# Kernel tuning notes

Hardware: AMD Instinct MI355X
Metric: run time of the kernel (lower is better)

The kernel has to match this reference:

```python
import jax, jax.numpy as jnp
import numpy as np

NBINS = (128, 64, 32)
LOG2PI = float(np.log(2.0 * np.pi))


def _quadratic_spline_stack(x, genes_oi, local_gene_ix, delta, uh, uw):
    """Stack of piecewise-quadratic (piecewise-linear density) splines on [0,1].
    Per split with n heights / n-1 widths (n-1 bins). Returns (outputs, logabsdet)."""
    uh_oi = uh[genes_oi]  # [G, sum(n)]
    uw_oi = uw[genes_oi]  # [G, sum(n-1)]
    outputs = x
    logabsdet = jnp.zeros_like(x)
    oh = ow = od = 0
    for n in NBINS:
        nh, nw = n, n - 1
        uhs = uh_oi[:, oh:oh + nh]
        uws = uw_oi[:, ow:ow + nw]
        ds = delta[:, od:od + nh]
        oh += nh; ow += nw; od += nh
        # per-gene bin widths / locations
        widths_g = jax.nn.softmax(uws, axis=-1)                     # [G, nw]
        bl = jnp.cumsum(widths_g, axis=-1)
        bl = bl.at[:, -1].set(1.0)
        bin_loc_g = jnp.pad(bl, ((0, 0), (1, 0)))                   # [G, nw+1]
        # gather per cut
        w = widths_g[local_gene_ix]                                 # [N, nw]
        loc = bin_loc_g[local_gene_ix]                              # [N, nw+1]
        # per-cut knot heights: gene baseline + cell/gene delta, normalized to unit area
        h_un = jnp.exp(uhs[local_gene_ix] + ds)                     # [N, nh]
        area = jnp.sum(0.5 * (h_un[:, :-1] + h_un[:, 1:]) * w, axis=-1, keepdims=True)
        h = h_un / area                                             # [N, nh]
        seg = 0.5 * (h[:, :-1] + h[:, 1:]) * w                      # bin masses [N, nw]
        left_cdf = jnp.pad(jnp.cumsum(seg, axis=-1)[:, :-1], ((0, 0), (1, 0)))  # [N, nw]
        # locate bin
        bin_idx = jnp.clip(jnp.sum(outputs[:, None] >= loc, axis=-1) - 1, 0, nw - 1)
        gi = bin_idx[:, None]
        loc_l = jnp.take_along_axis(loc, gi, -1)[:, 0]
        w_b = jnp.take_along_axis(w, gi, -1)[:, 0]
        cdf_l = jnp.take_along_axis(left_cdf, gi, -1)[:, 0]
        h_l = jnp.take_along_axis(h, gi, -1)[:, 0]
        h_r = jnp.take_along_axis(h, gi + 1, -1)[:, 0]
        alpha = (outputs - loc_l) / w_b
        outputs = (0.5 * (h_r - h_l) * w_b) * alpha * alpha + h_l * w_b * alpha + cdf_l
        logabsdet = logabsdet + jnp.log(h_l + (h_r - h_l) * alpha)
    return outputs, logabsdet


def setup_inputs() -> dict:
    key = jax.random.key(0)
    ks = jax.random.split(key, 10)
    B, L, G_total, G_oi, C, N = 512, 16, 20000, 500, 224, 200000
    clustering = jax.random.uniform(ks[0], (B, L), dtype=jnp.float32)
    coordinates = jax.random.uniform(ks[1], (N,), dtype=jnp.float32, minval=1e-4, maxval=1.0 - 1e-4)
    genes_oi = jax.random.randint(ks[2], (G_oi,), 0, G_total)
    local_gene_ix = jax.random.randint(ks[3], (N,), 0, G_oi)
    local_cellxgene_ix = jax.random.randint(ks[4], (N,), 0, B * G_oi)
    localcellxgene_ix = jax.random.randint(ks[5], (N,), 0, B * G_total)
    logit_weight = jax.random.normal(ks[6], (G_total, L, C), dtype=jnp.float32) * 0.01
    rho_weight = jax.random.normal(ks[7], (G_total, L), dtype=jnp.float32) * 0.05
    rho_bias = 1e-5 + (1.0 - 1e-5) * jax.random.uniform(ks[8], (G_total,), dtype=jnp.float32)
    k9, k10 = jax.random.split(ks[9])
    unnormalized_heights = jax.random.normal(k9, (G_total, sum(NBINS)), dtype=jnp.float32) * 0.1
    unnormalized_widths = jax.random.normal(k10, (G_total, sum(n - 1 for n in NBINS)), dtype=jnp.float32) * 0.1
    return dict(clustering=clustering, coordinates=coordinates, genes_oi=genes_oi,
                local_gene_ix=local_gene_ix, local_cellxgene_ix=local_cellxgene_ix,
                localcellxgene_ix=localcellxgene_ix, logit_weight=logit_weight,
                rho_weight=rho_weight, rho_bias=rho_bias,
                unnormalized_heights=unnormalized_heights,
                unnormalized_widths=unnormalized_widths)


def reference(clustering, coordinates, genes_oi, local_gene_ix, local_cellxgene_ix,
              localcellxgene_ix, logit_weight, rho_weight, rho_bias,
              unnormalized_heights, unnormalized_widths):
    B = clustering.shape[0]
    G = genes_oi.shape[0]
    n_total_genes = rho_bias.shape[0]
    # Decoder (n_layers=0 -> nn_output = latent)
    lw_oi = logit_weight[genes_oi]                                   # [G, L, C]
    mixture_delta = jnp.einsum('bl,glc->bgc', clustering, lw_oi)     # [B, G, C]
    rho_delta = clustering @ rho_weight.T                            # [B, G_total]
    rho = jax.nn.softmax(jnp.log(rho_bias)[None, :] + rho_delta, axis=-1)
    rho_cuts = rho.reshape(-1)[localcellxgene_ix]                    # [N]
    md_cuts = mixture_delta.reshape(B * G, -1)[local_cellxgene_ix]   # [N, C]
    _, lik_mixture = _quadratic_spline_stack(coordinates, genes_oi, local_gene_ix,
                                             md_cuts, unnormalized_heights, unnormalized_widths)
    lik_overall = jnp.log(rho_cuts) + jnp.log(jnp.float32(n_total_genes))
    elbo = -jnp.sum(lik_mixture + lik_overall)
    # Normal(0, exp(log_scale=0)=1) regularization log-probs
    def normal_logpdf(v):
        return -0.5 * v * v - 0.5 * LOG2PI
    elbo = elbo - jnp.sum(normal_logpdf(lw_oi))
    elbo = elbo - jnp.sum(normal_logpdf(rho_weight[genes_oi]))
    return elbo
```

## Files before the change

### kernel.cpp

```cpp
#include <hip/hip_runtime.h>
#include <cstddef>

#define LOG2PI_F 1.8378770664093453f

__device__ __forceinline__ float wave_sum(float v) {
#pragma unroll
    for (int o = 32; o >= 1; o >>= 1) v += __shfl_xor(v, o, 64);
    return v;
}
__device__ __forceinline__ float wave_max(float v) {
#pragma unroll
    for (int o = 32; o >= 1; o >>= 1) v = fmaxf(v, __shfl_xor(v, o, 64));
    return v;
}
__device__ __forceinline__ float wave_scan_incl(float v, int lane) {
#pragma unroll
    for (int o = 1; o < 64; o <<= 1) {
        float t = __shfl_up(v, o, 64);
        if (lane >= o) v += t;
    }
    return v;
}

__global__ void k_logrb(const float* __restrict__ rho_bias, float* __restrict__ logrb, int G_total) {
    int g = blockIdx.x * blockDim.x + threadIdx.x;
    if (g < G_total) logrb[g] = __logf(rho_bias[g]);
}

__global__ void k_prep_genes(const int* __restrict__ genes_oi,
                             const float* __restrict__ uh, const float* __restrict__ uw,
                             float4* __restrict__ pk, int G_oi) {
    const int g = blockIdx.x;
    const int t = threadIdx.x;
    const int gs = genes_oi[g];
    const float* uhg = uh + (size_t)gs * 224;
    const float* uwg = uw + (size_t)gs * 221;

    const int NH[3] = {128, 64, 32};
    const int OH[3] = {0, 128, 192};
    const int OW[3] = {0, 127, 190};
    const int SO[3] = {0, 128, 191};
#pragma unroll
    for (int lev = 0; lev < 3; ++lev) {
        const int nw = NH[lev] - 1;
        float v0 = (t < nw)      ? uwg[OW[lev] + t]      : -INFINITY;
        float v1 = (t + 64 < nw) ? uwg[OW[lev] + t + 64] : -INFINITY;
        float mx = wave_max(fmaxf(v0, v1));
        float e0 = (t < nw)      ? __expf(v0 - mx) : 0.f;
        float e1 = (t + 64 < nw) ? __expf(v1 - mx) : 0.f;
        float inv = 1.0f / wave_sum(e0 + e1);
        float w0 = e0 * inv, w1 = e1 * inv;
        float i0 = wave_scan_incl(w0, t);
        float tot0 = __shfl(i0, 63, 64);
        float i1 = wave_scan_incl(w1, t) + tot0;
        if (t < nw) {
            float loc = (t == nw - 1) ? 1.0f : i0;
            pk[(size_t)(SO[lev] + t) * G_oi + g] = make_float4(uhg[OH[lev] + t + 1], 0.5f * w0, loc, 0.f);
        }
        if (t + 64 < nw) {
            int j = t + 64;
            float loc = (j == nw - 1) ? 1.0f : i1;
            pk[(size_t)(SO[lev] + j) * G_oi + g] = make_float4(uhg[OH[lev] + j + 1], 0.5f * w1, loc, 0.f);
        }
    }
    if (t == 0) pk[(size_t)127 * G_oi + g] = make_float4(uhg[0], uhg[128], uhg[192], 0.f);
}

__global__ void k_prep_lwT(const int* __restrict__ genes_oi,
                           const float* __restrict__ lw, const float* __restrict__ rw,
                           float* __restrict__ lwT, float* __restrict__ pB) {
    const int g = blockIdx.x;
    const int tid = threadIdx.x;
    const int gs = genes_oi[g];
    const float* src = lw + (size_t)gs * 3584;
    float* dst = lwT + (size_t)g * 3584;
    float acc = 0.f;
    if (tid < 224) {
        float vv[16];
#pragma unroll
        for (int l = 0; l < 16; ++l) {
            float v = src[l * 224 + tid];
            vv[l] = v;
            acc = fmaf(v, v, acc);
        }
        float4* d4 = (float4*)(dst + (size_t)tid * 16);
#pragma unroll
        for (int q = 0; q < 4; ++q)
            d4[q] = make_float4(vv[4 * q + 0], vv[4 * q + 1], vv[4 * q + 2], vv[4 * q + 3]);
    }
    if (tid < 16) { float v = rw[(size_t)gs * 16 + tid]; acc = fmaf(v, v, acc); }
    __shared__ float sm[256];
    sm[tid] = acc;
    __syncthreads();
    for (int o = 128; o > 0; o >>= 1) { if (tid < o) sm[tid] += sm[tid + o]; __syncthreads(); }
    if (tid == 0) pB[g] = 0.5f * sm[0] + 0.5f * LOG2PI_F * (3584.0f + 16.0f);
}

__global__ void k_lse4(const float* __restrict__ clustering, const float* __restrict__ rw,
                       const float* __restrict__ logrb, float* __restrict__ lse,
                       int G_total, int B) {
    const int b0 = blockIdx.x * 4;
    const int tid = threadIdx.x;
    const int nc = min(4, B - b0);

    float cl[4][16];
#pragma unroll
    for (int c = 0; c < 4; ++c) {
        if (c < nc) {
            const float4* c4 = (const float4*)(clustering + (size_t)(b0 + c) * 16);
#pragma unroll
            for (int q = 0; q < 4; ++q) {
                float4 v = c4[q];
                cl[c][4 * q + 0] = v.x; cl[c][4 * q + 1] = v.y;
                cl[c][4 * q + 2] = v.z; cl[c][4 * q + 3] = v.w;
            }
        } else {
#pragma unroll
            for (int l = 0; l < 16; ++l) cl[c][l] = 0.f;
        }
    }

    float m[4], s[4];
#pragma unroll
    for (int c = 0; c < 4; ++c) { m[c] = -INFINITY; s[c] = 0.f; }

    for (int g = tid; g < G_total; g += 256) {
        const float4* r4 = (const float4*)(rw + (size_t)g * 16);
        float4 rv[4];
#pragma unroll
        for (int q = 0; q < 4; ++q) rv[q] = r4[q];
        const float lb = logrb[g];
#pragma unroll
        for (int c = 0; c < 4; ++c) {
            float d = 0.f;
#pragma unroll
            for (int q = 0; q < 4; ++q) {
                d = fmaf(cl[c][4 * q + 0], rv[q].x, d);
                d = fmaf(cl[c][4 * q + 1], rv[q].y, d);
                d = fmaf(cl[c][4 * q + 2], rv[q].z, d);
                d = fmaf(cl[c][4 * q + 3], rv[q].w, d);
            }
            float logit = lb + d;
            float mn = fmaxf(m[c], logit);
            s[c] = s[c] * __expf(m[c] - mn) + __expf(logit - mn);
            m[c] = mn;
        }
    }

    __shared__ float ms[4][256], ss[4][256];
#pragma unroll
    for (int c = 0; c < 4; ++c) { ms[c][tid] = m[c]; ss[c][tid] = s[c]; }
    __syncthreads();
    for (int o = 128; o > 0; o >>= 1) {
        if (tid < o) {
#pragma unroll
            for (int c = 0; c < 4; ++c) {
                float m2 = ms[c][tid + o], s2 = ss[c][tid + o];
                float mn = fmaxf(ms[c][tid], m2);
                ss[c][tid] = ss[c][tid] * __expf(ms[c][tid] - mn) + s2 * __expf(m2 - mn);
                ms[c][tid] = mn;
            }
        }
        __syncthreads();
    }
    if (tid < 4 && tid < nc) lse[b0 + tid] = ms[tid][0] + __logf(ss[tid][0]);
}

__global__ void k_zero(int* __restrict__ p, int n) {
    int i = blockIdx.x * blockDim.x + threadIdx.x;
    if (i < n) p[i] = 0;
}

__global__ void k_hist(const int* __restrict__ lcx, int* __restrict__ counts, int N, int G_oi) {
    int i = blockIdx.x * blockDim.x + threadIdx.x;
    if (i < N) atomicAdd(&counts[(unsigned)lcx[i] % (unsigned)G_oi], 1);
}

__global__ void k_scan(const int* __restrict__ counts, int* __restrict__ offsets,
                       int* __restrict__ cursor, int G_oi) {
    __shared__ int sm[512];
    const int t = threadIdx.x;
    int v = (t < G_oi) ? counts[t] : 0;
    sm[t] = v;
    __syncthreads();
    for (int o = 1; o < 512; o <<= 1) {
        int add = (t >= o) ? sm[t - o] : 0;
        __syncthreads();
        sm[t] += add;
        __syncthreads();
    }
    if (t < G_oi) {
        offsets[t + 1] = sm[t];
        cursor[t] = sm[t] - v;
    }
    if (t == 0) offsets[0] = 0;
}

__global__ void k_scatter(const float* __restrict__ coord, const int* __restrict__ lgix,
                          const int* __restrict__ lcx, const int* __restrict__ lc2,
                          int* __restrict__ cursor,
                          float* __restrict__ xs, int* __restrict__ b1s,
                          int* __restrict__ lc2s, int* __restrict__ ghs, int N, int G_oi) {
    int i = blockIdx.x * blockDim.x + threadIdx.x;
    if (i >= N) return;
    unsigned v = (unsigned)lcx[i];
    unsigned g = v % (unsigned)G_oi;
    int pos = atomicAdd(&cursor[g], 1);
    xs[pos]   = coord[i];
    b1s[pos]  = (int)(v / (unsigned)G_oi);
    lc2s[pos] = lc2[i];
    ghs[pos]  = lgix[i];
}

__launch_bounds__(512, 4)
__global__ void k_main2(const float* __restrict__ xs, const int* __restrict__ b1s,
                        const int* __restrict__ lc2s, const int* __restrict__ ghs,
                        const int* __restrict__ offsets,
                        const float* __restrict__ clustering,
                        const float* __restrict__ lwT,
                        const float4* __restrict__ pk,
                        const float* __restrict__ rw,
                        const float* __restrict__ logrb,
                        const float* __restrict__ lse,
                        float* __restrict__ pA, int G_oi, int G_total) {
    const int g = blockIdx.x;
    const int tid = threadIdx.x;
    const float* lwg = lwT + (size_t)g * 3584;
    const int s = offsets[g], e = offsets[g + 1];
    const float logGt = __logf((float)G_total);
    float acc = 0.f;

    __shared__ int   s_cnt[512];
    __shared__ int   s_cur[512];
    __shared__ float s_x[512];
    __shared__ int2  s_meta[512];
    __shared__ float wsm[8];

    for (int base = s; base < e; base += 512) {
        const int cnt = min(512, e - base);
        const int i = base + tid;
        const bool valid = tid < cnt;
        const int isafe = valid ? i : s;
        float x0   = xs[isafe];
        int   b1_0 = b1s[isafe];
        int   lc2_0= lc2s[isafe];
        int   gh_0 = ghs[isafe];

        s_cnt[tid] = 0;
        __syncthreads();
        if (valid) atomicAdd(&s_cnt[gh_0], 1);
        __syncthreads();
        int v = s_cnt[tid];
        for (int o = 1; o < 512; o <<= 1) {
            int add = (tid >= o) ? s_cnt[tid - o] : 0;
            __syncthreads();
            s_cnt[tid] += add;
            __syncthreads();
        }
        s_cur[tid] = s_cnt[tid] - v;
        __syncthreads();
        if (valid) {
            int pos = atomicAdd(&s_cur[gh_0], 1);
            s_x[pos]    = x0;
            s_meta[pos] = make_int2((b1_0 << 16) | gh_0, lc2_0);
        }
        __syncthreads();
        const int rd = valid ? tid : 0;
        float x  = s_x[rd];
        int2 mt  = s_meta[rd];
        const int gh  = mt.x & 0xffff;
        const int b1  = mt.x >> 16;
        const int lc2 = mt.y;

        float cl[16];
        {
            const float4* c4 = (const float4*)(clustering + (size_t)b1 * 16);
#pragma unroll
            for (int q = 0; q < 4; ++q) {
                float4 vv = c4[q];
                cl[4 * q + 0] = vv.x; cl[4 * q + 1] = vv.y; cl[4 * q + 2] = vv.z; cl[4 * q + 3] = vv.w;
            }
        }
        const float4 uh0 = pk[(size_t)127 * G_oi + gh];
        const float uh0v[3] = {uh0.x, uh0.y, uh0.z};

        float lad = 0.f;
        const int NH[3] = {128, 64, 32};
        const int OH[3] = {0, 128, 192};
        const int SO[3] = {0, 128, 191};
#pragma unroll
        for (int lev = 0; lev < 3; ++lev) {
            const int nw = NH[lev] - 1;
            const float* rowbase = lwg + (size_t)OH[lev] * 16;
            float hp;
            {
                float d = 0.f;
#pragma unroll
                for (int l = 0; l < 16; ++l) d = fmaf(cl[l], rowbase[l], d);
                hp = __expf(uh0v[lev] + d);
            }
            float h_l = hp, h_r = hp, whb = 0.f, loc_l = 0.f, cdf = 0.f, area = 0.f;
            int in = 0;
            const float4* pks = pk + (size_t)SO[lev] * G_oi + gh;
            for (int j = 0; j < nw; ++j) {
                const float* row = rowbase + (size_t)(j + 1) * 16;
                float d = 0.f;
#pragma unroll
                for (int l = 0; l < 16; ++l) d = fmaf(cl[l], row[l], d);
                float4 pkv = *pks;
                pks += G_oi;
                float hn = __expf(pkv.x + d);
                float seg = (hp + hn) * pkv.y;
                bool inJ = (in == j);
                if (inJ) { h_r = hn; whb = pkv.y; }
                bool adv = (x >= pkv.z) && (j < nw - 1);
                if (adv) { cdf += seg; h_l = hn; loc_l = pkv.z; in = j + 1; }
                area += seg;
                hp = hn;
            }
            float inv_area = __builtin_amdgcn_rcpf(area);
            float alpha = (x - loc_l) * 0.5f * __builtin_amdgcn_rcpf(whb);
            float t2 = whb * alpha;
            x = (t2 * fmaf(h_r - h_l, alpha, 2.f * h_l) + cdf) * inv_area;
            lad += __logf(fmaf(h_r - h_l, alpha, h_l)) - __logf(area);
        }

        unsigned b2 = (unsigned)lc2 / (unsigned)G_total;
        unsigned gt = (unsigned)lc2 - b2 * (unsigned)G_total;
        float d2 = 0.f;
        {
            const float4* c24 = (const float4*)(clustering + (size_t)b2 * 16);
            const float4* r4  = (const float4*)(rw + (size_t)gt * 16);
#pragma unroll
            for (int q = 0; q < 4; ++q) {
                float4 a = c24[q], b = r4[q];
                d2 = fmaf(a.x, b.x, d2); d2 = fmaf(a.y, b.y, d2);
                d2 = fmaf(a.z, b.z, d2); d2 = fmaf(a.w, b.w, d2);
            }
        }
        float lik = logrb[gt] + d2 - lse[b2] + logGt;
        if (valid) acc -= (lad + lik);
    }

    acc = wave_sum(acc);
    if ((tid & 63) == 0) wsm[tid >> 6] = acc;
    __syncthreads();
    if (tid == 0) {
        float t = 0.f;
#pragma unroll
        for (int w = 0; w < 8; ++w) t += wsm[w];
        pA[g] = t;
    }
}

__global__ void k_final(const float* __restrict__ pA, const float* __restrict__ pB,
                        float* __restrict__ out, int nA, int nB) {
    const int tid = threadIdx.x;
    float acc = 0.f;
    for (int i = tid; i < nA; i += blockDim.x) acc += pA[i];
    for (int i = tid; i < nB; i += blockDim.x) acc += pB[i];
    __shared__ float sm[256];
    sm[tid] = acc;
    __syncthreads();
    for (int o = 128; o > 0; o >>= 1) { if (tid < o) sm[tid] += sm[tid + o]; __syncthreads(); }
    if (tid == 0) out[0] = sm[0];
}

extern "C" void kernel_launch(void* const* d_in, const int* in_sizes, int n_in,
                              void* d_out, int out_size, void* d_ws, size_t ws_size,
                              hipStream_t stream) {
    const float* clustering        = (const float*)d_in[0];
    const float* coordinates       = (const float*)d_in[1];
    const int*   genes_oi          = (const int*)d_in[2];
    const int*   local_gene_ix     = (const int*)d_in[3];
    const int*   local_cellxgene_ix= (const int*)d_in[4];
    const int*   localcellxgene_ix = (const int*)d_in[5];
    const float* lw                = (const float*)d_in[6];
    const float* rw                = (const float*)d_in[7];
    const float* rho_bias          = (const float*)d_in[8];
    const float* uh                = (const float*)d_in[9];
    const float* uw                = (const float*)d_in[10];

    const int G_total = in_sizes[8];
    const int G_oi    = in_sizes[2];
    const int N       = in_sizes[1];
    const int L       = in_sizes[7] / G_total;
    const int B       = in_sizes[0] / L;

    size_t off = 0;
    char* base = (char*)d_ws;
    auto alloc = [&](size_t nbytes) {
        char* p = base + off;
        off = (off + nbytes + 15) & ~(size_t)15;
        return (void*)p;
    };
    float*  pA      = (float*)alloc(sizeof(float) * (G_oi + 16));
    float*  pB      = (float*)alloc(sizeof(float) * (G_oi + 16));
    float*  lse     = (float*)alloc(sizeof(float) * (B + 16));
    float*  logrb   = (float*)alloc(sizeof(float) * G_total);
    float*  lwT     = (float*)alloc(sizeof(float) * (size_t)G_oi * 3584);
    float4* pk      = (float4*)alloc(sizeof(float4) * (size_t)G_oi * 224);
    int*    counts  = (int*)alloc(sizeof(int) * 512);
    int*    offsets = (int*)alloc(sizeof(int) * 512);
    int*    cursor  = (int*)alloc(sizeof(int) * 512);
    float*  xs      = (float*)alloc(sizeof(float) * N);
    int*    b1s     = (int*)alloc(sizeof(int) * N);
    int*    lc2s    = (int*)alloc(sizeof(int) * N);
    int*    ghs     = (int*)alloc(sizeof(int) * N);
    (void)ws_size;

    const int TPB = 256;
    k_logrb<<<(G_total + TPB - 1) / TPB, TPB, 0, stream>>>(rho_bias, logrb, G_total);
    k_prep_genes<<<G_oi, 64, 0, stream>>>(genes_oi, uh, uw, pk, G_oi);
    k_prep_lwT<<<G_oi, 256, 0, stream>>>(genes_oi, lw, rw, lwT, pB);
    k_lse4<<<(B + 3) / 4, 256, 0, stream>>>(clustering, rw, logrb, lse, G_total, B);
    k_zero<<<2, 256, 0, stream>>>(counts, 512);
    k_hist<<<(N + TPB - 1) / TPB, TPB, 0, stream>>>(local_cellxgene_ix, counts, N, G_oi);
    k_scan<<<1, 512, 0, stream>>>(counts, offsets, cursor, G_oi);
    k_scatter<<<(N + TPB - 1) / TPB, TPB, 0, stream>>>(coordinates, local_gene_ix,
                                                       local_cellxgene_ix, localcellxgene_ix,
                                                       cursor, xs, b1s, lc2s, ghs, N, G_oi);
    k_main2<<<G_oi, 512, 0, stream>>>(xs, b1s, lc2s, ghs, offsets, clustering, lwT, pk,
                                      rw, logrb, lse, pA, G_oi, G_total);
    k_final<<<1, 256, 0, stream>>>(pA, pB, (float*)d_out, G_oi, G_oi);
}
```

Before: 647.6 us.

## Use packed FP32 FMAs, pack scattered cut data, and fuse small kernels

Rewrites the 16-wide dot products in the main spline loop and in the LSE kernel as two-lane `ext_vector_type` FMAs, so the compiler can emit packed FP32 instructions. The scatter step now writes one float4 per cut (x, packed b1/gene index, lc2) instead of four separate arrays, and the main kernel stages those float4s in LDS. Lanes with no cut now skip all work. Separately, the log of `rho_bias` is folded into the histogram kernel, zeroing of the counts moves into `k_prep_genes`, and `k_lse4` is launched later in the stream. The fused `logrb` write assumes N ≥ G_total and the bit packing assumes small index ranges.

```diff
diff --git a/kernel.cpp b/kernel.cpp
--- a/kernel.cpp
+++ b/kernel.cpp
@@ -2,6 +2,8 @@
 #include <cstddef>
 
 #define LOG2PI_F 1.8378770664093453f
+
+typedef float f2 __attribute__((ext_vector_type(2)));
 
 __device__ __forceinline__ float wave_sum(float v) {
 #pragma unroll
@@ -22,16 +24,19 @@
     return v;
 }
 
-__global__ void k_logrb(const float* __restrict__ rho_bias, float* __restrict__ logrb, int G_total) {
-    int g = blockIdx.x * blockDim.x + threadIdx.x;
-    if (g < G_total) logrb[g] = __logf(rho_bias[g]);
+__device__ __forceinline__ float dot16(const f2* __restrict__ a, const f2* __restrict__ b) {
+    f2 dv = a[0] * b[0];
+#pragma unroll
+    for (int l = 1; l < 8; ++l) dv = __builtin_elementwise_fma(a[l], b[l], dv);
+    return dv.x + dv.y;
 }
 
 __global__ void k_prep_genes(const int* __restrict__ genes_oi,
                              const float* __restrict__ uh, const float* __restrict__ uw,
-                             float4* __restrict__ pk, int G_oi) {
+                             float4* __restrict__ pk, int* __restrict__ counts, int G_oi) {
     const int g = blockIdx.x;
     const int t = threadIdx.x;
+    if (t == 0) counts[g] = 0;
     const int gs = genes_oi[g];
     const float* uhg = uh + (size_t)gs * 224;
     const float* uwg = uw + (size_t)gs * 221;
@@ -96,83 +101,11 @@
     if (tid == 0) pB[g] = 0.5f * sm[0] + 0.5f * LOG2PI_F * (3584.0f + 16.0f);
 }
 
-__global__ void k_lse4(const float* __restrict__ clustering, const float* __restrict__ rw,
-                       const float* __restrict__ logrb, float* __restrict__ lse,
-                       int G_total, int B) {
-    const int b0 = blockIdx.x * 4;
-    const int tid = threadIdx.x;
-    const int nc = min(4, B - b0);
-
-    float cl[4][16];
-#pragma unroll
-    for (int c = 0; c < 4; ++c) {
-        if (c < nc) {
-            const float4* c4 = (const float4*)(clustering + (size_t)(b0 + c) * 16);
-#pragma unroll
-            for (int q = 0; q < 4; ++q) {
-                float4 v = c4[q];
-                cl[c][4 * q + 0] = v.x; cl[c][4 * q + 1] = v.y;
-                cl[c][4 * q + 2] = v.z; cl[c][4 * q + 3] = v.w;
-            }
-        } else {
-#pragma unroll
-            for (int l = 0; l < 16; ++l) cl[c][l] = 0.f;
-        }
-    }
-
-    float m[4], s[4];
-#pragma unroll
-    for (int c = 0; c < 4; ++c) { m[c] = -INFINITY; s[c] = 0.f; }
-
-    for (int g = tid; g < G_total; g += 256) {
-        const float4* r4 = (const float4*)(rw + (size_t)g * 16);
-        float4 rv[4];
-#pragma unroll
-        for (int q = 0; q < 4; ++q) rv[q] = r4[q];
-        const float lb = logrb[g];
-#pragma unroll
-        for (int c = 0; c < 4; ++c) {
-            float d = 0.f;
-#pragma unroll
-            for (int q = 0; q < 4; ++q) {
-                d = fmaf(cl[c][4 * q + 0], rv[q].x, d);
-                d = fmaf(cl[c][4 * q + 1], rv[q].y, d);
-                d = fmaf(cl[c][4 * q + 2], rv[q].z, d);
-                d = fmaf(cl[c][4 * q + 3], rv[q].w, d);
-            }
-            float logit = lb + d;
-            float mn = fmaxf(m[c], logit);
-            s[c] = s[c] * __expf(m[c] - mn) + __expf(logit - mn);
-            m[c] = mn;
-        }
-    }
-
-    __shared__ float ms[4][256], ss[4][256];
-#pragma unroll
-    for (int c = 0; c < 4; ++c) { ms[c][tid] = m[c]; ss[c][tid] = s[c]; }
-    __syncthreads();
-    for (int o = 128; o > 0; o >>= 1) {
-        if (tid < o) {
-#pragma unroll
-            for (int c = 0; c < 4; ++c) {
-                float m2 = ms[c][tid + o], s2 = ss[c][tid + o];
-                float mn = fmaxf(ms[c][tid], m2);
-                ss[c][tid] = ss[c][tid] * __expf(ms[c][tid] - mn) + s2 * __expf(m2 - mn);
-                ms[c][tid] = mn;
-            }
-        }
-        __syncthreads();
-    }
-    if (tid < 4 && tid < nc) lse[b0 + tid] = ms[tid][0] + __logf(ss[tid][0]);
-}
-
-__global__ void k_zero(int* __restrict__ p, int n) {
+__global__ void k_hist_logrb(const int* __restrict__ lcx, int* __restrict__ counts,
+                             const float* __restrict__ rho_bias, float* __restrict__ logrb,
+                             int N, int G_oi, int G_total) {
     int i = blockIdx.x * blockDim.x + threadIdx.x;
-    if (i < n) p[i] = 0;
-}
-
-__global__ void k_hist(const int* __restrict__ lcx, int* __restrict__ counts, int N, int G_oi) {
-    int i = blockIdx.x * blockDim.x + threadIdx.x;
+    if (i < G_total) logrb[i] = __logf(rho_bias[i]);
     if (i < N) atomicAdd(&counts[(unsigned)lcx[i] % (unsigned)G_oi], 1);
 }
 
@@ -198,23 +131,86 @@
 
 __global__ void k_scatter(const float* __restrict__ coord, const int* __restrict__ lgix,
                           const int* __restrict__ lcx, const int* __restrict__ lc2,
-                          int* __restrict__ cursor,
-                          float* __restrict__ xs, int* __restrict__ b1s,
-                          int* __restrict__ lc2s, int* __restrict__ ghs, int N, int G_oi) {
+                          int* __restrict__ cursor, float4* __restrict__ xv, int N, int G_oi) {
     int i = blockIdx.x * blockDim.x + threadIdx.x;
     if (i >= N) return;
     unsigned v = (unsigned)lcx[i];
     unsigned g = v % (unsigned)G_oi;
     int pos = atomicAdd(&cursor[g], 1);
-    xs[pos]   = coord[i];
-    b1s[pos]  = (int)(v / (unsigned)G_oi);
-    lc2s[pos] = lc2[i];
-    ghs[pos]  = lgix[i];
+    int b1 = (int)(v / (unsigned)G_oi);
+    xv[pos] = make_float4(coord[i], __int_as_float((b1 << 16) | lgix[i]),
+                          __int_as_float(lc2[i]), 0.f);
+}
+
+__global__ void k_lse4(const float* __restrict__ clustering, const float* __restrict__ rw,
+                       const float* __restrict__ logrb, float* __restrict__ lse,
+                       int G_total, int B) {
+    const int b0 = blockIdx.x * 4;
+    const int tid = threadIdx.x;
+    const int nc = min(4, B - b0);
+
+    f2 cl[4][8];
+#pragma unroll
+    for (int c = 0; c < 4; ++c) {
+        if (c < nc) {
+            const float4* c4 = (const float4*)(clustering + (size_t)(b0 + c) * 16);
+#pragma unroll
+            for (int q = 0; q < 4; ++q) {
+                float4 v = c4[q];
+                cl[c][2 * q + 0] = (f2){v.x, v.y};
+                cl[c][2 * q + 1] = (f2){v.z, v.w};
+            }
+        } else {
+#pragma unroll
+            for (int l = 0; l < 8; ++l) cl[c][l] = (f2){0.f, 0.f};
+        }
+    }
+
+    float m[4], s[4];
+#pragma unroll
+    for (int c = 0; c < 4; ++c) { m[c] = -INFINITY; s[c] = 0.f; }
+
+    for (int g = tid; g < G_total; g += 256) {
+        const float4* r4 = (const float4*)(rw + (size_t)g * 16);
+        f2 rv[8];
+#pragma unroll
+        for (int q = 0; q < 4; ++q) {
+            float4 v = r4[q];
+            rv[2 * q + 0] = (f2){v.x, v.y};
+            rv[2 * q + 1] = (f2){v.z, v.w};
+        }
+        const float lb = logrb[g];
+#pragma unroll
+        for (int c = 0; c < 4; ++c) {
+            float d = dot16(cl[c], rv);
+            float logit = lb + d;
+            float mn = fmaxf(m[c], logit);
+            s[c] = s[c] * __expf(m[c] - mn) + __expf(logit - mn);
+            m[c] = mn;
+        }
+    }
+
+    __shared__ float ms[4][256], ss[4][256];
+#pragma unroll
+    for (int c = 0; c < 4; ++c) { ms[c][tid] = m[c]; ss[c][tid] = s[c]; }
+    __syncthreads();
+    for (int o = 128; o > 0; o >>= 1) {
+        if (tid < o) {
+#pragma unroll
+            for (int c = 0; c < 4; ++c) {
+                float m2 = ms[c][tid + o], s2 = ss[c][tid + o];
+                float mn = fmaxf(ms[c][tid], m2);
+                ss[c][tid] = ss[c][tid] * __expf(ms[c][tid] - mn) + s2 * __expf(m2 - mn);
+                ms[c][tid] = mn;
+            }
+        }
+        __syncthreads();
+    }
+    if (tid < 4 && tid < nc) lse[b0 + tid] = ms[tid][0] + __logf(ss[tid][0]);
 }
 
 __launch_bounds__(512, 4)
-__global__ void k_main2(const float* __restrict__ xs, const int* __restrict__ b1s,
-                        const int* __restrict__ lc2s, const int* __restrict__ ghs,
+__global__ void k_main2(const float4* __restrict__ xv,
                         const int* __restrict__ offsets,
                         const float* __restrict__ clustering,
                         const float* __restrict__ lwT,
@@ -230,21 +226,16 @@
     const float logGt = __logf((float)G_total);
     float acc = 0.f;
 
-    __shared__ int   s_cnt[512];
-    __shared__ int   s_cur[512];
-    __shared__ float s_x[512];
-    __shared__ int2  s_meta[512];
-    __shared__ float wsm[8];
+    __shared__ int    s_cnt[512];
+    __shared__ int    s_cur[512];
+    __shared__ float4 s_v[512];
+    __shared__ float  wsm[8];
 
     for (int base = s; base < e; base += 512) {
         const int cnt = min(512, e - base);
-        const int i = base + tid;
         const bool valid = tid < cnt;
-        const int isafe = valid ? i : s;
-        float x0   = xs[isafe];
-        int   b1_0 = b1s[isafe];
-        int   lc2_0= lc2s[isafe];
-        int   gh_0 = ghs[isafe];
+        float4 v0 = xv[valid ? base + tid : s];
+        const int gh_0 = __float_as_int(v0.y) & 0xffff;
 
         s_cnt[tid] = 0;
         __syncthreads();
@@ -261,85 +252,81 @@
         __syncthreads();
         if (valid) {
             int pos = atomicAdd(&s_cur[gh_0], 1);
-            s_x[pos]    = x0;
-            s_meta[pos] = make_int2((b1_0 << 16) | gh_0, lc2_0);
-        }
-        __syncthreads();
-        const int rd = valid ? tid : 0;
-        float x  = s_x[rd];
-        int2 mt  = s_meta[rd];
-        const int gh  = mt.x & 0xffff;
-        const int b1  = mt.x >> 16;
-        const int lc2 = mt.y;
-
-        float cl[16];
-        {
-            const float4* c4 = (const float4*)(clustering + (size_t)b1 * 16);
-#pragma unroll
-            for (int q = 0; q < 4; ++q) {
-                float4 vv = c4[q];
-                cl[4 * q + 0] = vv.x; cl[4 * q + 1] = vv.y; cl[4 * q + 2] = vv.z; cl[4 * q + 3] = vv.w;
+            s_v[pos] = v0;
+        }
+        __syncthreads();
+
+        if (valid) {
+            float4 vv = s_v[tid];
+            float x = vv.x;
+            const int meta = __float_as_int(vv.y);
+            const int gh  = meta & 0xffff;
+            const int b1  = meta >> 16;
+            const int lc2 = __float_as_int(vv.z);
+
+            f2 cl[8];
+            {
+                const float4* c4 = (const float4*)(clustering + (size_t)b1 * 16);
+#pragma unroll
+                for (int q = 0; q < 4; ++q) {
+                    float4 t4 = c4[q];
+                    cl[2 * q + 0] = (f2){t4.x, t4.y};
+                    cl[2 * q + 1] = (f2){t4.z, t4.w};
+                }
             }
-        }
-        const float4 uh0 = pk[(size_t)127 * G_oi + gh];
-        const float uh0v[3] = {uh0.x, uh0.y, uh0.z};
-
-        float lad = 0.f;
-        const int NH[3] = {128, 64, 32};
-        const int OH[3] = {0, 128, 192};
-        const int SO[3] = {0, 128, 191};
-#pragma unroll
-        for (int lev = 0; lev < 3; ++lev) {
-            const int nw = NH[lev] - 1;
-            const float* rowbase = lwg + (size_t)OH[lev] * 16;
-            float hp;
+            const float4 uh0 = pk[(size_t)127 * G_oi + gh];
+            const float uh0v[3] = {uh0.x, uh0.y, uh0.z};
+
+            float lad = 0.f;
+            const int NH[3] = {128, 64, 32};
+            const int OH[3] = {0, 128, 192};
+            const int SO[3] = {0, 128, 191};
+#pragma unroll
+            for (int lev = 0; lev < 3; ++lev) {
+                const int nw = NH[lev] - 1;
+                const float* rowbase = lwg + (size_t)OH[lev] * 16;
+                float hp = __expf(uh0v[lev] + dot16((const f2*)rowbase, cl));
+                float h_l = hp, h_r = hp, whb = 0.f, loc_l = 0.f, cdf = 0.f, area = 0.f;
+                int in = 0;
+                const float4* pks = pk + (size_t)SO[lev] * G_oi + gh;
+                for (int j = 0; j < nw; ++j) {
+                    const f2* row = (const f2*)(rowbase + (size_t)(j + 1) * 16);
+                    float d = dot16(row, cl);
+                    float4 pkv = *pks;
+                    pks += G_oi;
+                    float hn = __expf(pkv.x + d);
+                    float seg = (hp + hn) * pkv.y;
+                    bool inJ = (in == j);
+                    if (inJ) { h_r = hn; whb = pkv.y; }
+                    bool adv = (x >= pkv.z) && (j < nw - 1);
+                    if (adv) { cdf += seg; h_l = hn; loc_l = pkv.z; in = j + 1; }
+                    area += seg;
+                    hp = hn;
+                }
+                float inv_area = __builtin_amdgcn_rcpf(area);
+                float alpha = (x - loc_l) * 0.5f * __builtin_amdgcn_rcpf(whb);
+                float t2 = whb * alpha;
+                x = (t2 * fmaf(h_r - h_l, alpha, 2.f * h_l) + cdf) * inv_area;
+                lad += __logf(fmaf(h_r - h_l, alpha, h_l)) - __logf(area);
+            }
+
+            unsigned b2 = (unsigned)lc2 / (unsigned)G_total;
+            unsigned gt = (unsigned)lc2 - b2 * (unsigned)G_total;
+            f2 c2[8], r2[8];
             {
-                float d = 0.f;
-#pragma unroll
-                for (int l = 0; l < 16; ++l) d = fmaf(cl[l], rowbase[l], d);
-                hp = __expf(uh0v[lev] + d);
+                const float4* c24 = (const float4*)(clustering + (size_t)b2 * 16);
+                const float4* r4  = (const float4*)(rw + (size_t)gt * 16);
+#pragma unroll
+                for (int q = 0; q < 4; ++q) {
+                    float4 a = c24[q], b = r4[q];
+                    c2[2 * q + 0] = (f2){a.x, a.y}; c2[2 * q + 1] = (f2){a.z, a.w};
+                    r2[2 * q + 0] = (f2){b.x, b.y}; r2[2 * q + 1] = (f2){b.z, b.w};
+                }
             }
-            float h_l = hp, h_r = hp, whb = 0.f, loc_l = 0.f, cdf = 0.f, area = 0.f;
-            int in = 0;
-            const float4* pks = pk + (size_t)SO[lev] * G_oi + gh;
-            for (int j = 0; j < nw; ++j) {
-                const float* row = rowbase + (size_t)(j + 1) * 16;
-                float d = 0.f;
-#pragma unroll
-                for (int l = 0; l < 16; ++l) d = fmaf(cl[l], row[l], d);
-                float4 pkv = *pks;
-                pks += G_oi;
-                float hn = __expf(pkv.x + d);
-                float seg = (hp + hn) * pkv.y;
-                bool inJ = (in == j);
-                if (inJ) { h_r = hn; whb = pkv.y; }
-                bool adv = (x >= pkv.z) && (j < nw - 1);
-                if (adv) { cdf += seg; h_l = hn; loc_l = pkv.z; in = j + 1; }
-                area += seg;
-                hp = hn;
-            }
-            float inv_area = __builtin_amdgcn_rcpf(area);
-            float alpha = (x - loc_l) * 0.5f * __builtin_amdgcn_rcpf(whb);
-            float t2 = whb * alpha;
-            x = (t2 * fmaf(h_r - h_l, alpha, 2.f * h_l) + cdf) * inv_area;
-            lad += __logf(fmaf(h_r - h_l, alpha, h_l)) - __logf(area);
-        }
-
-        unsigned b2 = (unsigned)lc2 / (unsigned)G_total;
-        unsigned gt = (unsigned)lc2 - b2 * (unsigned)G_total;
-        float d2 = 0.f;
-        {
-            const float4* c24 = (const float4*)(clustering + (size_t)b2 * 16);
-            const float4* r4  = (const float4*)(rw + (size_t)gt * 16);
-#pragma unroll
-            for (int q = 0; q < 4; ++q) {
-                float4 a = c24[q], b = r4[q];
-                d2 = fmaf(a.x, b.x, d2); d2 = fmaf(a.y, b.y, d2);
-                d2 = fmaf(a.z, b.z, d2); d2 = fmaf(a.w, b.w, d2);
-            }
-        }
-        float lik = logrb[gt] + d2 - lse[b2] + logGt;
-        if (valid) acc -= (lad + lik);
+            float d2 = dot16(c2, r2);
+            float lik = logrb[gt] + d2 - lse[b2] + logGt;
+            acc -= (lad + lik);
+        }
     }
 
     acc = wave_sum(acc);
@@ -403,24 +390,20 @@
     int*    counts  = (int*)alloc(sizeof(int) * 512);
     int*    offsets = (int*)alloc(sizeof(int) * 512);
     int*    cursor  = (int*)alloc(sizeof(int) * 512);
-    float*  xs      = (float*)alloc(sizeof(float) * N);
-    int*    b1s     = (int*)alloc(sizeof(int) * N);
-    int*    lc2s    = (int*)alloc(sizeof(int) * N);
-    int*    ghs     = (int*)alloc(sizeof(int) * N);
+    float4* xv      = (float4*)alloc(sizeof(float4) * (size_t)N);
     (void)ws_size;
 
     const int TPB = 256;
-    k_logrb<<<(G_total + TPB - 1) / TPB, TPB, 0, stream>>>(rho_bias, logrb, G_total);
-    k_prep_genes<<<G_oi, 64, 0, stream>>>(genes_oi, uh, uw, pk, G_oi);
+    k_prep_genes<<<G_oi, 64, 0, stream>>>(genes_oi, uh, uw, pk, counts, G_oi);
     k_prep_lwT<<<G_oi, 256, 0, stream>>>(genes_oi, lw, rw, lwT, pB);
-    k_lse4<<<(B + 3) / 4, 256, 0, stream>>>(clustering, rw, logrb, lse, G_total, B);
-    k_zero<<<2, 256, 0, stream>>>(counts, 512);
-    k_hist<<<(N + TPB - 1) / TPB, TPB, 0, stream>>>(local_cellxgene_ix, counts, N, G_oi);
+    k_hist_logrb<<<(N + TPB - 1) / TPB, TPB, 0, stream>>>(local_cellxgene_ix, counts,
+                                                          rho_bias, logrb, N, G_oi, G_total);
     k_scan<<<1, 512, 0, stream>>>(counts, offsets, cursor, G_oi);
     k_scatter<<<(N + TPB - 1) / TPB, TPB, 0, stream>>>(coordinates, local_gene_ix,
                                                        local_cellxgene_ix, localcellxgene_ix,
-                                                       cursor, xs, b1s, lc2s, ghs, N, G_oi);
-    k_main2<<<G_oi, 512, 0, stream>>>(xs, b1s, lc2s, ghs, offsets, clustering, lwT, pk,
+                                                       cursor, xv, N, G_oi);
+    k_lse4<<<(B + 3) / 4, 256, 0, stream>>>(clustering, rw, logrb, lse, G_total, B);
+    k_main2<<<G_oi, 512, 0, stream>>>(xv, offsets, clustering, lwT, pk,
                                       rw, logrb, lse, pA, G_oi, G_total);
     k_final<<<1, 256, 0, stream>>>(pA, pB, (float*)d_out, G_oi, G_oi);
 }
```

Measured after the change: 633.4 us. -2.2%, faster.
